# Optimization experiments

Measured on AMD Instinct MI355X. Metric: run time of the kernel, lower is better.

Reference implementation:

```python
import jax, jax.numpy as jnp
import numpy as np

B, S, D = 2, 2048, 1024
H, DK = 16, 64  # num_heads, key_dim (value_dim defaults to key_dim)


def setup_inputs() -> dict:
    key = jax.random.key(0)
    ks = jax.random.split(key, 11)
    init = lambda k, shape, fan_in: jax.random.uniform(
        k, shape, jnp.float32, -1.0, 1.0) * (1.0 / np.sqrt(fan_in))
    return {
        "query": jax.random.normal(ks[0], (B, S, D), jnp.float32),
        "key": jax.random.normal(ks[1], (B, S, D), jnp.float32),
        "value": jax.random.normal(ks[2], (B, S, D), jnp.float32),
        "Wq": init(ks[3], (D, H, DK), D),
        "bq": jnp.zeros((H, DK), jnp.float32),
        "Wk": init(ks[4], (D, H, DK), D),
        "bk": jnp.zeros((H, DK), jnp.float32),
        "Wv": init(ks[5], (D, H, DK), D),
        "bv": jnp.zeros((H, DK), jnp.float32),
        "Wo": init(ks[6], (H, DK, D), H * DK),
        "bo": jnp.zeros((D,), jnp.float32),
    }


def reference(query, key, value, Wq, bq, Wk, bk, Wv, bv, Wo, bo):
    # QKV projections: abc,cde->abde (EinsumDense with bias on (H, DK))
    q = jnp.einsum("bsd,dhk->bshk", query, Wq) + bq  # [B,S,H,DK]
    k = jnp.einsum("bsd,dhk->bshk", key, Wk) + bk
    v = jnp.einsum("bsd,dhk->bshk", value, Wv) + bv
    # Keras scales the query before the dot product
    q = q * (1.0 / jnp.sqrt(jnp.asarray(DK, q.dtype)))
    # aecd,abcd->acbe : [B,H,Sq,Sk]
    scores = jnp.einsum("bqhk,bshk->bhqs", q, k)
    probs = jax.nn.softmax(scores, axis=-1)
    # acbe,aecd->abcd : [B,Sq,H,DK]
    attn = jnp.einsum("bhqs,bshk->bqhk", probs, v)
    # output projection: abcd,cde->abe
    out = jnp.einsum("bqhk,hkd->bqd", attn, Wo) + bo  # [B,S,D]
    return out
```

## Files before the change

kernel.cpp:

```cpp
#include <hip/hip_runtime.h>
#include <hip/hip_bf16.h>
#include <stdint.h>
#include <stddef.h>


typedef __bf16 bf16;
typedef __attribute__((ext_vector_type(4))) bf16 bf16x4;
typedef __attribute__((ext_vector_type(8))) bf16 bf16x8;
typedef __attribute__((ext_vector_type(4))) float f32x4;
typedef __attribute__((ext_vector_type(16))) float f32x16;
typedef __attribute__((ext_vector_type(2))) unsigned int uint2v;

#define DEVINL static __device__ __forceinline__

DEVINL void gload_lds16(const void* g, void* l) {
  __builtin_amdgcn_global_load_lds(
      (const __attribute__((address_space(1))) void*)g,
      (__attribute__((address_space(3))) void*)l, 16, 0, 0);
}

DEVINL f32x4 mfma16(bf16x8 a, bf16x8 b, f32x4 c) {
  return __builtin_amdgcn_mfma_f32_16x16x32_bf16(a, b, c, 0, 0, 0);
}
DEVINL f32x16 mfma32(bf16x8 a, bf16x8 b, f32x16 c) {
  return __builtin_amdgcn_mfma_f32_32x32x16_bf16(a, b, c, 0, 0, 0);
}
DEVINL float fexp2(float x) {
  float r;
  asm("v_exp_f32 %0, %1" : "=v"(r) : "v"(x));
  return r;
}
DEVINL unsigned pack2(float lo, float hi) {
  union { bf16 h[2]; unsigned u; } t;
  t.h[0] = (bf16)lo; t.h[1] = (bf16)hi;
  return t.u;
}
DEVINL bf16x8 mk8(unsigned a, unsigned b, unsigned c, unsigned d) {
  union { unsigned u[4]; bf16x8 v; } t;
  t.u[0] = a; t.u[1] = b; t.u[2] = c; t.u[3] = d;
  return t.v;
}

__global__ __launch_bounds__(256) void wt_kernel(
    const float* __restrict__ w0, const float* __restrict__ w1,
    const float* __restrict__ w2, const float* __restrict__ w3,
    bf16* __restrict__ out) {
  __shared__ float tile[64 * 65];
  int t = blockIdx.y;
  const float* w = (t == 0) ? w0 : (t == 1) ? w1 : (t == 2) ? w2 : w3;
  bf16* o = out + (size_t)t * 1024 * 1024;
  int tb = blockIdx.x;
  int k0 = (tb >> 4) * 64, n0 = (tb & 15) * 64;
  int c = threadIdx.x & 63, r0 = threadIdx.x >> 6;
  for (int r = r0; r < 64; r += 4)
    tile[r * 65 + c] = w[(size_t)(k0 + r) * 1024 + n0 + c];
  __syncthreads();
  for (int r = r0; r < 64; r += 4)
    o[(size_t)(n0 + r) * 1024 + k0 + c] = (bf16)tile[c * 65 + r];
}

__global__ __launch_bounds__(256) void gemm_qkv(
    const float* __restrict__ Aq, const float* __restrict__ Ak,
    const float* __restrict__ Av, const bf16* __restrict__ Wt,
    const float* __restrict__ bq, const float* __restrict__ bk,
    const float* __restrict__ bv,
    bf16* __restrict__ outQ, bf16* __restrict__ outK, bf16* __restrict__ Vt) {
  int z = blockIdx.z;
  const float* A   = (z == 0) ? Aq : (z == 1) ? Ak : Av;
  const bf16* Wz   = Wt + (size_t)z * 1024 * 1024;
  const float* bia = (z == 0) ? bq : (z == 1) ? bk : bv;
  float scale      = (z == 0) ? 0.18033688011112042f : 1.0f;

  __shared__ float Af[2][128 * 32];
  __shared__ bf16  Bs[2][128 * 32];

  int m0 = blockIdx.x * 128, n0 = blockIdx.y * 128;
  int tid = threadIdx.x, w = tid >> 6, l = tid & 63;
  int wm = (w >> 1) * 64, wn = (w & 1) * 64;
  int c16 = l & 15, g = l >> 4;
  int rsw = (c16 >> 1) & 3;

  int ua[4], arow[4], asrc[4];
#pragma unroll
  for (int i = 0; i < 4; ++i) {
    ua[i] = (w * 4 + i) * 64 + l;
    arow[i] = ua[i] >> 3;
    asrc[i] = ((ua[i] & 7) ^ (arow[i] & 7)) * 4;
  }
  int brow0 = (w * 2 + 0) * 16 + (l >> 2);
  int brow1 = (w * 2 + 1) * 16 + (l >> 2);
  int bk0 = ((l & 3) ^ ((brow0 >> 1) & 3)) * 8;
  int bk1 = ((l & 3) ^ ((brow1 >> 1) & 3)) * 8;

  f32x4 acc[4][4] = {};

#define STAGE_QKV(buf, kt)                                                   \
  do {                                                                       \
    _Pragma("unroll") for (int i = 0; i < 4; ++i)                            \
      gload_lds16(A + (size_t)(m0 + arow[i]) * 1024 + (kt) + asrc[i],        \
                  (char*)Af[buf] + ua[i] * 16);                              \
    gload_lds16(Wz + (size_t)(n0 + brow0) * 1024 + (kt) + bk0,               \
                (char*)Bs[buf] + (w * 2 + 0) * 1024 + l * 16);               \
    gload_lds16(Wz + (size_t)(n0 + brow1) * 1024 + (kt) + bk1,               \
                (char*)Bs[buf] + (w * 2 + 1) * 1024 + l * 16);               \
  } while (0)

  STAGE_QKV(0, 0);
  __syncthreads();

  int cur = 0;
  for (int kt = 0; kt < 1024; kt += 32) {
    if (kt < 992) STAGE_QKV(cur ^ 1, kt + 32);
    bf16x8 af[4], bfr[4];
#pragma unroll
    for (int mt = 0; mt < 4; ++mt) {
      int row = wm + mt * 16 + c16;
      int r7 = row & 7;
      f32x4 lo = *(const f32x4*)&Af[cur][row * 32 + (((2 * g)     ^ r7) << 2)];
      f32x4 hi = *(const f32x4*)&Af[cur][row * 32 + (((2 * g + 1) ^ r7) << 2)];
      bf16x8 h;
#pragma unroll
      for (int j = 0; j < 4; ++j) { h[j] = (bf16)lo[j]; h[4 + j] = (bf16)hi[j]; }
      af[mt] = h;
    }
#pragma unroll
    for (int nt = 0; nt < 4; ++nt)
      bfr[nt] = *(const bf16x8*)&Bs[cur][(wn + nt * 16 + c16) * 32 + ((g ^ rsw) * 8)];
#pragma unroll
    for (int mt = 0; mt < 4; ++mt)
#pragma unroll
      for (int nt = 0; nt < 4; ++nt)
        acc[mt][nt] = mfma16(af[mt], bfr[nt], acc[mt][nt]);
    __syncthreads();
    cur ^= 1;
  }
#undef STAGE_QKV

  if (z < 2) {
    bf16* Cout = (z == 0) ? outQ : outK;
#pragma unroll
    for (int mt = 0; mt < 4; ++mt)
#pragma unroll
      for (int nt = 0; nt < 4; ++nt) {
        int n = n0 + wn + nt * 16 + c16;
        float bb = bia[n];
#pragma unroll
        for (int r = 0; r < 4; ++r) {
          int m = m0 + wm + mt * 16 + g * 4 + r;
          Cout[(size_t)m * 1024 + n] = (bf16)((acc[mt][nt][r] + bb) * scale);
        }
      }
  } else {
#pragma unroll
    for (int mt = 0; mt < 4; ++mt)
#pragma unroll
      for (int nt = 0; nt < 4; ++nt) {
        int n = n0 + wn + nt * 16 + c16;
        float bb = bia[n];
        int m = m0 + wm + mt * 16 + g * 4;
        int b = m >> 11, s = m & 2047;
        bf16x4 v;
#pragma unroll
        for (int r = 0; r < 4; ++r) v[r] = (bf16)(acc[mt][nt][r] + bb);
        *(bf16x4*)&Vt[((size_t)(b * 16 + (n >> 6)) * 64 + (n & 63)) * 2048 + s] = v;
      }
  }
}

__global__ __launch_bounds__(256) void flash_kernel(
    const bf16* __restrict__ Qp, const bf16* __restrict__ Kp,
    const bf16* __restrict__ Vt, bf16* __restrict__ AO) {
  __shared__ __align__(16) bf16 Ks[4][64 * 64];
  __shared__ __align__(16) bf16 Vs[4][64 * 64];

  int orig = blockIdx.x;
  int wg = (orig & 7) * 64 + (orig >> 3);
  int bh = wg >> 4, qb = wg & 15;
  int b = bh >> 4, h = bh & 15;
  int tid = threadIdx.x, w = tid >> 6, l = tid & 63;
  int lo5 = l & 31, g = l >> 5;
  int q0 = qb * 128 + w * 32;

  const bf16* qptr = Qp + (size_t)(b * 2048 + q0 + lo5) * 1024 + h * 64 + g * 8;
  bf16x8 qf0 = *(const bf16x8*)(qptr + 0);
  bf16x8 qf1 = *(const bf16x8*)(qptr + 16);
  bf16x8 qf2 = *(const bf16x8*)(qptr + 32);
  bf16x8 qf3 = *(const bf16x8*)(qptr + 48);

  const bf16* kbase = Kp + (size_t)(b * 2048) * 1024 + h * 64;
  const bf16* vbase = Vt + (size_t)bh * 64 * 2048;

  int u0 = w * 64 + l;
  int u1 = (4 + w) * 64 + l;
  int r0s = u0 >> 3, c0s = (u0 & 7) ^ (r0s & 7);
  int r1s = u1 >> 3, c1s = (u1 & 7) ^ (r1s & 7);

#define STAGE(buf, s0)                                                          \
  do {                                                                          \
    gload_lds16(kbase + (size_t)((s0) + r0s) * 1024 + c0s * 8,                  \
                (bf16*)Ks[buf] + u0 * 8);                                       \
    gload_lds16(kbase + (size_t)((s0) + r1s) * 1024 + c1s * 8,                  \
                (bf16*)Ks[buf] + u1 * 8);                                       \
    gload_lds16(vbase + (size_t)r0s * 2048 + (s0) + c0s * 8,                    \
                (bf16*)Vs[buf] + u0 * 8);                                       \
    gload_lds16(vbase + (size_t)r1s * 2048 + (s0) + c1s * 8,                    \
                (bf16*)Vs[buf] + u1 * 8);                                       \
  } while (0)

#define LDSK(cp, nt, kt) \
  (*(const bf16x8*)&cp[(((nt)*32 + lo5) << 6) + (((((kt)*2 + g)) ^ (lo5 & 7)) << 3)])
#define LDSV(cp, dt, st) \
  (*(const bf16x8*)&cp[(((dt)*32 + lo5) << 6) + (((((st)*2 + g)) ^ (lo5 & 7)) << 3)])

  f32x16 o0 = {}, o1 = {};
  float ps0 = 0.f, ps1 = 0.f, ps2 = 0.f, ps3 = 0.f;

  STAGE(0, 0);
  STAGE(1, 64);
  for (int t = 0; t < 32; ++t) {
    if (t < 30) {
      STAGE((t + 2) & 3, (t + 2) * 64);
      asm volatile("s_waitcnt vmcnt(8)" ::: "memory");
    } else if (t == 30) {
      asm volatile("s_waitcnt vmcnt(4)" ::: "memory");
    } else {
      asm volatile("s_waitcnt vmcnt(0)" ::: "memory");
    }
    __builtin_amdgcn_s_barrier();
    __builtin_amdgcn_sched_barrier(0);
    const bf16* kc = Ks[t & 3];
    const bf16* vc = Vs[t & 3];

    f32x16 sv = {}, sw = {};
    __builtin_amdgcn_s_setprio(1);
    sv = mfma32(LDSK(kc, 0, 0), qf0, sv);
    sv = mfma32(LDSK(kc, 0, 1), qf1, sv);
    sv = mfma32(LDSK(kc, 0, 2), qf2, sv);
    sv = mfma32(LDSK(kc, 0, 3), qf3, sv);
    sw = mfma32(LDSK(kc, 1, 0), qf0, sw);
    sw = mfma32(LDSK(kc, 1, 1), qf1, sw);
    sw = mfma32(LDSK(kc, 1, 2), qf2, sw);
    sw = mfma32(LDSK(kc, 1, 3), qf3, sw);
    __builtin_amdgcn_s_setprio(0);

    float p[16];
#pragma unroll
    for (int r = 0; r < 16; ++r) p[r] = fexp2(sv[r]);
    ps0 += p[0] + p[4] + p[8] + p[12];
    ps1 += p[1] + p[5] + p[9] + p[13];
    ps2 += p[2] + p[6] + p[10] + p[14];
    ps3 += p[3] + p[7] + p[11] + p[15];
    unsigned pw0 = pack2(p[0], p[1]), pw1 = pack2(p[2], p[3]);
    unsigned pw2 = pack2(p[4], p[5]), pw3 = pack2(p[6], p[7]);
    unsigned pw4 = pack2(p[8], p[9]), pw5 = pack2(p[10], p[11]);
    unsigned pw6 = pack2(p[12], p[13]), pw7 = pack2(p[14], p[15]);
    uint2v a02 = __builtin_amdgcn_permlane32_swap(pw0, pw2, false, false);
    uint2v a13 = __builtin_amdgcn_permlane32_swap(pw1, pw3, false, false);
    uint2v a46 = __builtin_amdgcn_permlane32_swap(pw4, pw6, false, false);
    uint2v a57 = __builtin_amdgcn_permlane32_swap(pw5, pw7, false, false);
    bf16x8 pa0 = mk8(a02.x, a13.x, a02.y, a13.y);
    bf16x8 pa1 = mk8(a46.x, a57.x, a46.y, a57.y);

#pragma unroll
    for (int r = 0; r < 16; ++r) p[r] = fexp2(sw[r]);
    ps0 += p[0] + p[4] + p[8] + p[12];
    ps1 += p[1] + p[5] + p[9] + p[13];
    ps2 += p[2] + p[6] + p[10] + p[14];
    ps3 += p[3] + p[7] + p[11] + p[15];
    pw0 = pack2(p[0], p[1]); pw1 = pack2(p[2], p[3]);
    pw2 = pack2(p[4], p[5]); pw3 = pack2(p[6], p[7]);
    pw4 = pack2(p[8], p[9]); pw5 = pack2(p[10], p[11]);
    pw6 = pack2(p[12], p[13]); pw7 = pack2(p[14], p[15]);
    a02 = __builtin_amdgcn_permlane32_swap(pw0, pw2, false, false);
    a13 = __builtin_amdgcn_permlane32_swap(pw1, pw3, false, false);
    a46 = __builtin_amdgcn_permlane32_swap(pw4, pw6, false, false);
    a57 = __builtin_amdgcn_permlane32_swap(pw5, pw7, false, false);
    bf16x8 pb0 = mk8(a02.x, a13.x, a02.y, a13.y);
    bf16x8 pb1 = mk8(a46.x, a57.x, a46.y, a57.y);

    __builtin_amdgcn_s_setprio(1);
    o0 = mfma32(pa0, LDSV(vc, 0, 0), o0);
    o1 = mfma32(pa0, LDSV(vc, 1, 0), o1);
    o0 = mfma32(pa1, LDSV(vc, 0, 1), o0);
    o1 = mfma32(pa1, LDSV(vc, 1, 1), o1);
    o0 = mfma32(pb0, LDSV(vc, 0, 2), o0);
    o1 = mfma32(pb0, LDSV(vc, 1, 2), o1);
    o0 = mfma32(pb1, LDSV(vc, 0, 3), o0);
    o1 = mfma32(pb1, LDSV(vc, 1, 3), o1);
    __builtin_amdgcn_s_setprio(0);
    __builtin_amdgcn_sched_barrier(0);
  }
#undef STAGE
#undef LDSK
#undef LDSV

  float plsum = (ps0 + ps1) + (ps2 + ps3);
  float tot = plsum + __shfl_xor(plsum, 32);

#pragma unroll
  for (int r = 0; r < 16; ++r) {
    int qr = (r & 3) + 8 * (r >> 2) + 4 * g;
    float inv = 1.0f / __shfl(tot, qr);
    bf16* op = AO + (size_t)(b * 2048 + q0 + qr) * 1024 + h * 64 + lo5;
    op[0]  = (bf16)(o0[r] * inv);
    op[32] = (bf16)(o1[r] * inv);
  }
}

__global__ __launch_bounds__(256) void gemm_o(
    const bf16* __restrict__ A, const bf16* __restrict__ Wt3,
    const float* __restrict__ bo, float* __restrict__ C) {
  __shared__ bf16 As[2][64 * 32];
  __shared__ bf16 Bs[2][128 * 32];
  int m0 = blockIdx.x * 64, n0 = blockIdx.y * 128;
  int tid = threadIdx.x, w = tid >> 6, l = tid & 63;
  int wm = (w >> 1) * 32, wn = (w & 1) * 64;
  int c16 = l & 15, g = l >> 4;
  int rsw = (c16 >> 1) & 3;

  int arow = tid >> 2, akc = tid & 3;
  int asrc = (akc ^ ((arow >> 1) & 3)) * 8;
  int brow0 = (w * 2 + 0) * 16 + (l >> 2);
  int brow1 = (w * 2 + 1) * 16 + (l >> 2);
  int bk0 = ((l & 3) ^ ((brow0 >> 1) & 3)) * 8;
  int bk1 = ((l & 3) ^ ((brow1 >> 1) & 3)) * 8;

  f32x4 acc[2][4] = {};

#define STAGE_O(buf, kt)                                                     \
  do {                                                                       \
    gload_lds16(A + (size_t)(m0 + arow) * 1024 + (kt) + asrc,                \
                (char*)As[buf] + tid * 16);                                  \
    gload_lds16(Wt3 + (size_t)(n0 + brow0) * 1024 + (kt) + bk0,              \
                (char*)Bs[buf] + (w * 2 + 0) * 1024 + l * 16);               \
    gload_lds16(Wt3 + (size_t)(n0 + brow1) * 1024 + (kt) + bk1,              \
                (char*)Bs[buf] + (w * 2 + 1) * 1024 + l * 16);               \
  } while (0)

  STAGE_O(0, 0);
  __syncthreads();

  int cur = 0;
  for (int kt = 0; kt < 1024; kt += 32) {
    if (kt < 992) STAGE_O(cur ^ 1, kt + 32);
    bf16x8 af[2], bfr[4];
#pragma unroll
    for (int mt = 0; mt < 2; ++mt)
      af[mt] = *(const bf16x8*)&As[cur][(wm + mt * 16 + c16) * 32 + ((g ^ rsw) * 8)];
#pragma unroll
    for (int nt = 0; nt < 4; ++nt)
      bfr[nt] = *(const bf16x8*)&Bs[cur][(wn + nt * 16 + c16) * 32 + ((g ^ rsw) * 8)];
#pragma unroll
    for (int mt = 0; mt < 2; ++mt)
#pragma unroll
      for (int nt = 0; nt < 4; ++nt)
        acc[mt][nt] = mfma16(af[mt], bfr[nt], acc[mt][nt]);
    __syncthreads();
    cur ^= 1;
  }
#undef STAGE_O

#pragma unroll
  for (int mt = 0; mt < 2; ++mt)
#pragma unroll
    for (int nt = 0; nt < 4; ++nt) {
      int n = n0 + wn + nt * 16 + c16;
      float bb = bo[n];
#pragma unroll
      for (int r = 0; r < 4; ++r) {
        int m = m0 + wm + mt * 16 + g * 4 + r;
        C[(size_t)m * 1024 + n] = acc[mt][nt][r] + bb;
      }
    }
}

extern "C" void kernel_launch(void* const* d_in, const int* in_sizes, int n_in,
                              void* d_out, int out_size, void* d_ws, size_t ws_size,
                              hipStream_t stream) {
  const float* query = (const float*)d_in[0];
  const float* key_  = (const float*)d_in[1];
  const float* value = (const float*)d_in[2];
  const float* Wq = (const float*)d_in[3];
  const float* bq = (const float*)d_in[4];
  const float* Wk = (const float*)d_in[5];
  const float* bk = (const float*)d_in[6];
  const float* Wv = (const float*)d_in[7];
  const float* bv = (const float*)d_in[8];
  const float* Wo = (const float*)d_in[9];
  const float* bo = (const float*)d_in[10];
  float* out = (float*)d_out;

  char* ws = (char*)d_ws;
  const size_t MB = 1024 * 1024;
  bf16* Wt  = (bf16*)(ws);
  bf16* Qp  = (bf16*)(ws + 8 * MB);
  bf16* Kp  = (bf16*)(ws + 16 * MB);
  bf16* Vt  = (bf16*)(ws + 24 * MB);
  bf16* AO  = (bf16*)(ws + 32 * MB);

  dim3 blk(256);
  wt_kernel<<<dim3(256, 4), blk, 0, stream>>>(Wq, Wk, Wv, Wo, Wt);
  gemm_qkv<<<dim3(32, 8, 3), blk, 0, stream>>>(query, key_, value, Wt,
                                               bq, bk, bv, Qp, Kp, Vt);
  flash_kernel<<<dim3(512), blk, 0, stream>>>(Qp, Kp, Vt, AO);
  gemm_o<<<dim3(64, 8), blk, 0, stream>>>(AO, Wt + (size_t)3 * 1024 * 1024, bo, out);
}
```

Before: 131.9 us.

## Shrink flash blocks to two waves with double-buffered K/V and more workgroups

```diff
diff --git a/kernel.cpp b/kernel.cpp
--- a/kernel.cpp
+++ b/kernel.cpp
@@ -167,19 +167,19 @@
   }
 }
 
-__global__ __launch_bounds__(256) void flash_kernel(
+__global__ __launch_bounds__(128) void flash_kernel(
     const bf16* __restrict__ Qp, const bf16* __restrict__ Kp,
     const bf16* __restrict__ Vt, bf16* __restrict__ AO) {
-  __shared__ __align__(16) bf16 Ks[4][64 * 64];
-  __shared__ __align__(16) bf16 Vs[4][64 * 64];
+  __shared__ __align__(16) bf16 Ks[2][64 * 64];
+  __shared__ __align__(16) bf16 Vs[2][64 * 64];
 
   int orig = blockIdx.x;
-  int wg = (orig & 7) * 64 + (orig >> 3);
-  int bh = wg >> 4, qb = wg & 15;
+  int wg = (orig & 7) * 128 + (orig >> 3);
+  int bh = wg >> 5, qb = wg & 31;
   int b = bh >> 4, h = bh & 15;
   int tid = threadIdx.x, w = tid >> 6, l = tid & 63;
   int lo5 = l & 31, g = l >> 5;
-  int q0 = qb * 128 + w * 32;
+  int q0 = qb * 64 + w * 32;
 
   const bf16* qptr = Qp + (size_t)(b * 2048 + q0 + lo5) * 1024 + h * 64 + g * 8;
   bf16x8 qf0 = *(const bf16x8*)(qptr + 0);
@@ -190,21 +190,22 @@
   const bf16* kbase = Kp + (size_t)(b * 2048) * 1024 + h * 64;
   const bf16* vbase = Vt + (size_t)bh * 64 * 2048;
 
-  int u0 = w * 64 + l;
-  int u1 = (4 + w) * 64 + l;
-  int r0s = u0 >> 3, c0s = (u0 & 7) ^ (r0s & 7);
-  int r1s = u1 >> 3, c1s = (u1 & 7) ^ (r1s & 7);
+  int uu[4], rs[4], cs[4];
+#pragma unroll
+  for (int i = 0; i < 4; ++i) {
+    uu[i] = i * 128 + tid;
+    rs[i] = uu[i] >> 3;
+    cs[i] = (uu[i] & 7) ^ (rs[i] & 7);
+  }
 
 #define STAGE(buf, s0)                                                          \
   do {                                                                          \
-    gload_lds16(kbase + (size_t)((s0) + r0s) * 1024 + c0s * 8,                  \
-                (bf16*)Ks[buf] + u0 * 8);                                       \
-    gload_lds16(kbase + (size_t)((s0) + r1s) * 1024 + c1s * 8,                  \
-                (bf16*)Ks[buf] + u1 * 8);                                       \
-    gload_lds16(vbase + (size_t)r0s * 2048 + (s0) + c0s * 8,                    \
-                (bf16*)Vs[buf] + u0 * 8);                                       \
-    gload_lds16(vbase + (size_t)r1s * 2048 + (s0) + c1s * 8,                    \
-                (bf16*)Vs[buf] + u1 * 8);                                       \
+    _Pragma("unroll") for (int i = 0; i < 4; ++i)                               \
+      gload_lds16(kbase + (size_t)((s0) + rs[i]) * 1024 + cs[i] * 8,            \
+                  (bf16*)Ks[buf] + uu[i] * 8);                                  \
+    _Pragma("unroll") for (int i = 0; i < 4; ++i)                               \
+      gload_lds16(vbase + (size_t)rs[i] * 2048 + (s0) + cs[i] * 8,              \
+                  (bf16*)Vs[buf] + uu[i] * 8);                                  \
   } while (0)
 
 #define LDSK(cp, nt, kt) \
@@ -216,33 +217,26 @@
   float ps0 = 0.f, ps1 = 0.f, ps2 = 0.f, ps3 = 0.f;
 
   STAGE(0, 0);
-  STAGE(1, 64);
+  int cur = 0;
   for (int t = 0; t < 32; ++t) {
-    if (t < 30) {
-      STAGE((t + 2) & 3, (t + 2) * 64);
+    if (t < 31) {
+      STAGE(cur ^ 1, (t + 1) * 64);
       asm volatile("s_waitcnt vmcnt(8)" ::: "memory");
-    } else if (t == 30) {
-      asm volatile("s_waitcnt vmcnt(4)" ::: "memory");
     } else {
       asm volatile("s_waitcnt vmcnt(0)" ::: "memory");
     }
     __builtin_amdgcn_s_barrier();
     __builtin_amdgcn_sched_barrier(0);
-    const bf16* kc = Ks[t & 3];
-    const bf16* vc = Vs[t & 3];
-
-    f32x16 sv = {}, sw = {};
+    const bf16* kc = Ks[cur];
+    const bf16* vc = Vs[cur];
+
+    f32x16 sv = {};
     __builtin_amdgcn_s_setprio(1);
     sv = mfma32(LDSK(kc, 0, 0), qf0, sv);
     sv = mfma32(LDSK(kc, 0, 1), qf1, sv);
     sv = mfma32(LDSK(kc, 0, 2), qf2, sv);
     sv = mfma32(LDSK(kc, 0, 3), qf3, sv);
-    sw = mfma32(LDSK(kc, 1, 0), qf0, sw);
-    sw = mfma32(LDSK(kc, 1, 1), qf1, sw);
-    sw = mfma32(LDSK(kc, 1, 2), qf2, sw);
-    sw = mfma32(LDSK(kc, 1, 3), qf3, sw);
     __builtin_amdgcn_s_setprio(0);
-
     float p[16];
 #pragma unroll
     for (int r = 0; r < 16; ++r) p[r] = fexp2(sv[r]);
@@ -261,6 +255,13 @@
     bf16x8 pa0 = mk8(a02.x, a13.x, a02.y, a13.y);
     bf16x8 pa1 = mk8(a46.x, a57.x, a46.y, a57.y);
 
+    f32x16 sw = {};
+    __builtin_amdgcn_s_setprio(1);
+    sw = mfma32(LDSK(kc, 1, 0), qf0, sw);
+    sw = mfma32(LDSK(kc, 1, 1), qf1, sw);
+    sw = mfma32(LDSK(kc, 1, 2), qf2, sw);
+    sw = mfma32(LDSK(kc, 1, 3), qf3, sw);
+    __builtin_amdgcn_s_setprio(0);
 #pragma unroll
     for (int r = 0; r < 16; ++r) p[r] = fexp2(sw[r]);
     ps0 += p[0] + p[4] + p[8] + p[12];
@@ -288,7 +289,10 @@
     o0 = mfma32(pb1, LDSV(vc, 0, 3), o0);
     o1 = mfma32(pb1, LDSV(vc, 1, 3), o1);
     __builtin_amdgcn_s_setprio(0);
+
     __builtin_amdgcn_sched_barrier(0);
+    __builtin_amdgcn_s_barrier();
+    cur ^= 1;
   }
 #undef STAGE
 #undef LDSK
@@ -398,10 +402,9 @@
   bf16* Vt  = (bf16*)(ws + 24 * MB);
   bf16* AO  = (bf16*)(ws + 32 * MB);
 
-  dim3 blk(256);
-  wt_kernel<<<dim3(256, 4), blk, 0, stream>>>(Wq, Wk, Wv, Wo, Wt);
-  gemm_qkv<<<dim3(32, 8, 3), blk, 0, stream>>>(query, key_, value, Wt,
-                                               bq, bk, bv, Qp, Kp, Vt);
-  flash_kernel<<<dim3(512), blk, 0, stream>>>(Qp, Kp, Vt, AO);
-  gemm_o<<<dim3(64, 8), blk, 0, stream>>>(AO, Wt + (size_t)3 * 1024 * 1024, bo, out);
-}
+  wt_kernel<<<dim3(256, 4), dim3(256), 0, stream>>>(Wq, Wk, Wv, Wo, Wt);
+  gemm_qkv<<<dim3(32, 8, 3), dim3(256), 0, stream>>>(query, key_, value, Wt,
+                                                     bq, bk, bv, Qp, Kp, Vt);
+  flash_kernel<<<dim3(1024), dim3(128), 0, stream>>>(Qp, Kp, Vt, AO);
+  gemm_o<<<dim3(64, 8), dim3(256), 0, stream>>>(AO, Wt + (size_t)3 * 1024 * 1024, bo, out);
+}
```

Result: slower. 134.8 us (+2.3%).

## Software-pipeline QK of next tile with softmax and PV of current tile

Applied to the files above, without the earlier changes.

```diff
diff --git a/kernel.cpp b/kernel.cpp
--- a/kernel.cpp
+++ b/kernel.cpp
@@ -167,7 +167,7 @@
   }
 }
 
-__global__ __launch_bounds__(256) void flash_kernel(
+__global__ __launch_bounds__(256, 2) void flash_kernel(
     const bf16* __restrict__ Qp, const bf16* __restrict__ Kp,
     const bf16* __restrict__ Vt, bf16* __restrict__ AO) {
   __shared__ __align__(16) bf16 Ks[4][64 * 64];
@@ -212,87 +212,114 @@
 #define LDSV(cp, dt, st) \
   (*(const bf16x8*)&cp[(((dt)*32 + lo5) << 6) + (((((st)*2 + g)) ^ (lo5 & 7)) << 3)])
 
-  f32x16 o0 = {}, o1 = {};
+#define QK(d0, d1, kc)                                                          \
+  do {                                                                          \
+    __builtin_amdgcn_s_setprio(1);                                              \
+    d0 = z16; d1 = z16;                                                         \
+    d0 = mfma32(LDSK(kc, 0, 0), qf0, d0);                                       \
+    d0 = mfma32(LDSK(kc, 0, 1), qf1, d0);                                       \
+    d0 = mfma32(LDSK(kc, 0, 2), qf2, d0);                                       \
+    d0 = mfma32(LDSK(kc, 0, 3), qf3, d0);                                       \
+    d1 = mfma32(LDSK(kc, 1, 0), qf0, d1);                                       \
+    d1 = mfma32(LDSK(kc, 1, 1), qf1, d1);                                       \
+    d1 = mfma32(LDSK(kc, 1, 2), qf2, d1);                                       \
+    d1 = mfma32(LDSK(kc, 1, 3), qf3, d1);                                       \
+    __builtin_amdgcn_s_setprio(0);                                              \
+  } while (0)
+
+#define SOFTMAX(sv, sw)                                                         \
+  do {                                                                          \
+    float p[16];                                                                \
+    _Pragma("unroll") for (int r = 0; r < 16; ++r) p[r] = fexp2(sv[r]);         \
+    ps0 += p[0] + p[4] + p[8] + p[12];                                          \
+    ps1 += p[1] + p[5] + p[9] + p[13];                                          \
+    ps2 += p[2] + p[6] + p[10] + p[14];                                         \
+    ps3 += p[3] + p[7] + p[11] + p[15];                                         \
+    unsigned pw0 = pack2(p[0], p[1]), pw1 = pack2(p[2], p[3]);                  \
+    unsigned pw2 = pack2(p[4], p[5]), pw3 = pack2(p[6], p[7]);                  \
+    unsigned pw4 = pack2(p[8], p[9]), pw5 = pack2(p[10], p[11]);                \
+    unsigned pw6 = pack2(p[12], p[13]), pw7 = pack2(p[14], p[15]);              \
+    uint2v a02 = __builtin_amdgcn_permlane32_swap(pw0, pw2, false, false);      \
+    uint2v a13 = __builtin_amdgcn_permlane32_swap(pw1, pw3, false, false);      \
+    uint2v a46 = __builtin_amdgcn_permlane32_swap(pw4, pw6, false, false);      \
+    uint2v a57 = __builtin_amdgcn_permlane32_swap(pw5, pw7, false, false);      \
+    pa0 = mk8(a02.x, a13.x, a02.y, a13.y);                                      \
+    pa1 = mk8(a46.x, a57.x, a46.y, a57.y);                                      \
+    _Pragma("unroll") for (int r = 0; r < 16; ++r) p[r] = fexp2(sw[r]);         \
+    ps0 += p[0] + p[4] + p[8] + p[12];                                          \
+    ps1 += p[1] + p[5] + p[9] + p[13];                                          \
+    ps2 += p[2] + p[6] + p[10] + p[14];                                         \
+    ps3 += p[3] + p[7] + p[11] + p[15];                                         \
+    pw0 = pack2(p[0], p[1]); pw1 = pack2(p[2], p[3]);                           \
+    pw2 = pack2(p[4], p[5]); pw3 = pack2(p[6], p[7]);                           \
+    pw4 = pack2(p[8], p[9]); pw5 = pack2(p[10], p[11]);                         \
+    pw6 = pack2(p[12], p[13]); pw7 = pack2(p[14], p[15]);                       \
+    a02 = __builtin_amdgcn_permlane32_swap(pw0, pw2, false, false);             \
+    a13 = __builtin_amdgcn_permlane32_swap(pw1, pw3, false, false);             \
+    a46 = __builtin_amdgcn_permlane32_swap(pw4, pw6, false, false);             \
+    a57 = __builtin_amdgcn_permlane32_swap(pw5, pw7, false, false);             \
+    pb0 = mk8(a02.x, a13.x, a02.y, a13.y);                                      \
+    pb1 = mk8(a46.x, a57.x, a46.y, a57.y);                                      \
+  } while (0)
+
+#define PV(vc)                                                                  \
+  do {                                                                          \
+    __builtin_amdgcn_s_setprio(1);                                              \
+    o0 = mfma32(pa0, LDSV(vc, 0, 0), o0);                                       \
+    o1 = mfma32(pa0, LDSV(vc, 1, 0), o1);                                       \
+    o0 = mfma32(pa1, LDSV(vc, 0, 1), o0);                                       \
+    o1 = mfma32(pa1, LDSV(vc, 1, 1), o1);                                       \
+    o0 = mfma32(pb0, LDSV(vc, 0, 2), o0);                                       \
+    o1 = mfma32(pb0, LDSV(vc, 1, 2), o1);                                       \
+    o0 = mfma32(pb1, LDSV(vc, 0, 3), o0);                                       \
+    o1 = mfma32(pb1, LDSV(vc, 1, 3), o1);                                       \
+    __builtin_amdgcn_s_setprio(0);                                              \
+  } while (0)
+
+  const f32x16 z16 = {};
+  f32x16 o0 = z16, o1 = z16;
+  f32x16 sA0, sA1, sB0, sB1;
+  bf16x8 pa0, pa1, pb0, pb1;
   float ps0 = 0.f, ps1 = 0.f, ps2 = 0.f, ps3 = 0.f;
 
   STAGE(0, 0);
   STAGE(1, 64);
-  for (int t = 0; t < 32; ++t) {
+  asm volatile("s_waitcnt vmcnt(6)" ::: "memory");
+  __builtin_amdgcn_s_barrier();
+  __builtin_amdgcn_sched_barrier(0);
+  QK(sA0, sA1, Ks[0]);
+
+  for (int t = 0; t < 32; t += 2) {
     if (t < 30) {
       STAGE((t + 2) & 3, (t + 2) * 64);
-      asm volatile("s_waitcnt vmcnt(8)" ::: "memory");
-    } else if (t == 30) {
-      asm volatile("s_waitcnt vmcnt(4)" ::: "memory");
+      asm volatile("s_waitcnt vmcnt(6)" ::: "memory");
+    } else {
+      asm volatile("s_waitcnt vmcnt(2)" ::: "memory");
+    }
+    __builtin_amdgcn_s_barrier();
+    __builtin_amdgcn_sched_barrier(0);
+    QK(sB0, sB1, Ks[(t + 1) & 3]);
+    SOFTMAX(sA0, sA1);
+    PV(Vs[t & 3]);
+
+    if (t < 29) {
+      STAGE((t + 3) & 3, (t + 3) * 64);
+      asm volatile("s_waitcnt vmcnt(6)" ::: "memory");
     } else {
       asm volatile("s_waitcnt vmcnt(0)" ::: "memory");
     }
     __builtin_amdgcn_s_barrier();
     __builtin_amdgcn_sched_barrier(0);
-    const bf16* kc = Ks[t & 3];
-    const bf16* vc = Vs[t & 3];
-
-    f32x16 sv = {}, sw = {};
-    __builtin_amdgcn_s_setprio(1);
-    sv = mfma32(LDSK(kc, 0, 0), qf0, sv);
-    sv = mfma32(LDSK(kc, 0, 1), qf1, sv);
-    sv = mfma32(LDSK(kc, 0, 2), qf2, sv);
-    sv = mfma32(LDSK(kc, 0, 3), qf3, sv);
-    sw = mfma32(LDSK(kc, 1, 0), qf0, sw);
-    sw = mfma32(LDSK(kc, 1, 1), qf1, sw);
-    sw = mfma32(LDSK(kc, 1, 2), qf2, sw);
-    sw = mfma32(LDSK(kc, 1, 3), qf3, sw);
-    __builtin_amdgcn_s_setprio(0);
-
-    float p[16];
-#pragma unroll
-    for (int r = 0; r < 16; ++r) p[r] = fexp2(sv[r]);
-    ps0 += p[0] + p[4] + p[8] + p[12];
-    ps1 += p[1] + p[5] + p[9] + p[13];
-    ps2 += p[2] + p[6] + p[10] + p[14];
-    ps3 += p[3] + p[7] + p[11] + p[15];
-    unsigned pw0 = pack2(p[0], p[1]), pw1 = pack2(p[2], p[3]);
-    unsigned pw2 = pack2(p[4], p[5]), pw3 = pack2(p[6], p[7]);
-    unsigned pw4 = pack2(p[8], p[9]), pw5 = pack2(p[10], p[11]);
-    unsigned pw6 = pack2(p[12], p[13]), pw7 = pack2(p[14], p[15]);
-    uint2v a02 = __builtin_amdgcn_permlane32_swap(pw0, pw2, false, false);
-    uint2v a13 = __builtin_amdgcn_permlane32_swap(pw1, pw3, false, false);
-    uint2v a46 = __builtin_amdgcn_permlane32_swap(pw4, pw6, false, false);
-    uint2v a57 = __builtin_amdgcn_permlane32_swap(pw5, pw7, false, false);
-    bf16x8 pa0 = mk8(a02.x, a13.x, a02.y, a13.y);
-    bf16x8 pa1 = mk8(a46.x, a57.x, a46.y, a57.y);
-
-#pragma unroll
-    for (int r = 0; r < 16; ++r) p[r] = fexp2(sw[r]);
-    ps0 += p[0] + p[4] + p[8] + p[12];
-    ps1 += p[1] + p[5] + p[9] + p[13];
-    ps2 += p[2] + p[6] + p[10] + p[14];
-    ps3 += p[3] + p[7] + p[11] + p[15];
-    pw0 = pack2(p[0], p[1]); pw1 = pack2(p[2], p[3]);
-    pw2 = pack2(p[4], p[5]); pw3 = pack2(p[6], p[7]);
-    pw4 = pack2(p[8], p[9]); pw5 = pack2(p[10], p[11]);
-    pw6 = pack2(p[12], p[13]); pw7 = pack2(p[14], p[15]);
-    a02 = __builtin_amdgcn_permlane32_swap(pw0, pw2, false, false);
-    a13 = __builtin_amdgcn_permlane32_swap(pw1, pw3, false, false);
-    a46 = __builtin_amdgcn_permlane32_swap(pw4, pw6, false, false);
-    a57 = __builtin_amdgcn_permlane32_swap(pw5, pw7, false, false);
-    bf16x8 pb0 = mk8(a02.x, a13.x, a02.y, a13.y);
-    bf16x8 pb1 = mk8(a46.x, a57.x, a46.y, a57.y);
-
-    __builtin_amdgcn_s_setprio(1);
-    o0 = mfma32(pa0, LDSV(vc, 0, 0), o0);
-    o1 = mfma32(pa0, LDSV(vc, 1, 0), o1);
-    o0 = mfma32(pa1, LDSV(vc, 0, 1), o0);
-    o1 = mfma32(pa1, LDSV(vc, 1, 1), o1);
-    o0 = mfma32(pb0, LDSV(vc, 0, 2), o0);
-    o1 = mfma32(pb0, LDSV(vc, 1, 2), o1);
-    o0 = mfma32(pb1, LDSV(vc, 0, 3), o0);
-    o1 = mfma32(pb1, LDSV(vc, 1, 3), o1);
-    __builtin_amdgcn_s_setprio(0);
-    __builtin_amdgcn_sched_barrier(0);
+    if (t < 30) QK(sA0, sA1, Ks[(t + 2) & 3]);
+    SOFTMAX(sB0, sB1);
+    PV(Vs[(t + 1) & 3]);
   }
 #undef STAGE
 #undef LDSK
 #undef LDSV
+#undef QK
+#undef SOFTMAX
+#undef PV
 
   float plsum = (ps0 + ps1) + (ps2 + ps3);
   float tot = plsum + __shfl_xor(plsum, 32);
@@ -398,10 +425,9 @@
   bf16* Vt  = (bf16*)(ws + 24 * MB);
   bf16* AO  = (bf16*)(ws + 32 * MB);
 
-  dim3 blk(256);
-  wt_kernel<<<dim3(256, 4), blk, 0, stream>>>(Wq, Wk, Wv, Wo, Wt);
-  gemm_qkv<<<dim3(32, 8, 3), blk, 0, stream>>>(query, key_, value, Wt,
-                                               bq, bk, bv, Qp, Kp, Vt);
-  flash_kernel<<<dim3(512), blk, 0, stream>>>(Qp, Kp, Vt, AO);
-  gemm_o<<<dim3(64, 8), blk, 0, stream>>>(AO, Wt + (size_t)3 * 1024 * 1024, bo, out);
-}
+  wt_kernel<<<dim3(256, 4), dim3(256), 0, stream>>>(Wq, Wk, Wv, Wo, Wt);
+  gemm_qkv<<<dim3(32, 8, 3), dim3(256), 0, stream>>>(query, key_, value, Wt,
+                                                     bq, bk, bv, Qp, Kp, Vt);
+  flash_kernel<<<dim3(512), dim3(256), 0, stream>>>(Qp, Kp, Vt, AO);
+  gemm_o<<<dim3(64, 8), dim3(256), 0, stream>>>(AO, Wt + (size_t)3 * 1024 * 1024, bo, out);
+}
```

After: 124.6 us. -5.5%, faster.
